# Optimization experiments

Measured on AMD Instinct MI355X. Metric: run time of the kernel, lower is better.

Reference implementation:

```python
import jax, jax.numpy as jnp
import numpy as np

B, S, H, NH = 2, 2048, 1024, 16
HD = H // NH  # head_dim = 64


def setup_inputs() -> dict:
    key = jax.random.key(0)
    kx, kl, kq, kk, kv, ko = jax.random.split(key, 6)
    scale = 1.0 / np.sqrt(H)
    return {
        "x": jax.random.normal(kx, (B, S, H), dtype=jnp.float32),
        "seq_lengths": jax.random.randint(kl, (B,), 1, S + 1, dtype=jnp.int32),
        "Wq": jax.random.normal(kq, (H, H), dtype=jnp.float32) * scale,
        "Wk": jax.random.normal(kk, (H, H), dtype=jnp.float32) * scale,
        "Wv": jax.random.normal(kv, (H, H), dtype=jnp.float32) * scale,
        "Wo": jax.random.normal(ko, (H, H), dtype=jnp.float32) * scale,
    }


def reference(x, seq_lengths, Wq, Wk, Wv, Wo):
    b, s, _ = x.shape
    # projections (nn.Linear with no bias: x @ W.T)
    q = (x @ Wq.T).reshape(b, s, NH, HD).transpose(0, 2, 1, 3)  # [b,h,s,d]
    k = (x @ Wk.T).reshape(b, s, NH, HD).transpose(0, 2, 1, 3)
    v = (x @ Wv.T).reshape(b, s, NH, HD).transpose(0, 2, 1, 3)

    scores = jnp.einsum("bhqd,bhkd->bhqk", q, k) / jnp.sqrt(jnp.float32(HD))

    causal = jnp.triu(jnp.ones((s, s), dtype=bool), k=1)[None, None]  # [1,1,s,s]
    padding = (jnp.arange(s)[None, :] >= seq_lengths[:, None])[:, None, None, :]
    mask = causal | padding
    scores = jnp.where(mask, -jnp.inf, scores)

    att = jax.nn.softmax(scores, axis=-1)  # stable: subtract row max once
    out = jnp.einsum("bhqk,bhkd->bhqd", att, v)
    out = out.transpose(0, 2, 1, 3).reshape(b, s, H)
    return out @ Wo.T
```

## Files before the change

### kernel.cpp

```cpp
#include <hip/hip_runtime.h>

typedef unsigned short u16;
typedef short bf16x8 __attribute__((ext_vector_type(8)));
typedef float f32x4 __attribute__((ext_vector_type(4)));

#define DEVINL __device__ __forceinline__

DEVINL u16 f2bf(float f) {
    union { float f; unsigned int u; } x;
    x.f = f;
    unsigned int u = x.u;
    unsigned int r = (u + 0x7fffu + ((u >> 16) & 1u)) >> 16;
    return (u16)r;
}

DEVINL unsigned int cvtpk(float a, float b) {
    unsigned int r;
    asm("v_cvt_pk_bf16_f32 %0, %1, %2" : "=v"(r) : "v"(a), "v"(b));
    return r;
}

DEVINL void async16(const u16* g, u16* l) {
    __builtin_amdgcn_global_load_lds(
        (const __attribute__((address_space(1))) void*)g,
        (__attribute__((address_space(3))) void*)l, 16, 0, 0);
}

DEVINL f32x4 mfma32(bf16x8 a, bf16x8 b, f32x4 c) {
    return __builtin_amdgcn_mfma_f32_16x16x32_bf16(a, b, c, 0, 0, 0);
}

__global__ void pma_cvt_all(const float* __restrict__ x,
                            const float* __restrict__ w0, const float* __restrict__ w1,
                            const float* __restrict__ w2, const float* __restrict__ w3,
                            u16* __restrict__ xb, u16* __restrict__ wdst) {
    const int y = blockIdx.y;
    const int i = blockIdx.x * 256 + threadIdx.x;
    const float4* src;
    ushort4* dst;
    float s = 1.0f;
    if (y < 4) {
        src = (const float4*)x + (size_t)y * 262144;
        dst = (ushort4*)xb + (size_t)y * 262144;
    } else {
        const int wsel = y - 4;
        const float* w = (wsel == 0) ? w0 : (wsel == 1) ? w1 : (wsel == 2) ? w2 : w3;
        src = (const float4*)w;
        dst = (ushort4*)wdst + (size_t)wsel * 262144;
        if (wsel == 0) s = 0.125f;
    }
    float4 v = src[i];
    ushort4 o;
    o.x = f2bf(v.x * s); o.y = f2bf(v.y * s); o.z = f2bf(v.z * s); o.w = f2bf(v.w * s);
    dst[i] = o;
}

__global__ __launch_bounds__(256) void pma_gemm_qkv(
    const u16* __restrict__ A,
    const u16* __restrict__ W0, const u16* __restrict__ W1, const u16* __restrict__ W2,
    u16* __restrict__ O0, u16* __restrict__ O1, u16* __restrict__ Vt,
    const int* __restrict__ seq_lengths)
{
    const int t = threadIdx.x;
    const int lane = t & 63, wave = t >> 6;
    const int m0 = blockIdx.x * 64;
    const int bn = blockIdx.y;
    const int which = bn >> 4;
    const int n0 = (bn & 15) * 64;

    if (which != 0 && (m0 & 2047) >= seq_lengths[m0 >> 11]) return;

    const u16* W = (which == 0) ? W0 : (which == 1) ? W1 : W2;

    __shared__ u16 Alds[64 * 64];
    __shared__ u16 Blds[64 * 64];

    const int wm = wave >> 1, wn = wave & 1;
    const int r16 = lane & 15, g4 = lane >> 4;
    const int r7 = r16 & 7;

    f32x4 acc[2][2];
    const f32x4 z = {0.f, 0.f, 0.f, 0.f};
#pragma unroll
    for (int m = 0; m < 2; ++m)
#pragma unroll
        for (int n = 0; n < 2; ++n) acc[m][n] = z;

    for (int k0 = 0; k0 < 1024; k0 += 64) {
        __syncthreads();
#pragma unroll
        for (int j = 0; j < 2; ++j) {
            int i = j * 256 + t;
            int row = i >> 3, seg = i & 7;
            int sc = ((seg ^ (row & 7)) * 8);
            async16(A + (size_t)(m0 + row) * 1024 + k0 + sc,
                    Alds + (size_t)(j * 256 + wave * 64) * 8);
            async16(W + (size_t)(n0 + row) * 1024 + k0 + sc,
                    Blds + (size_t)(j * 256 + wave * 64) * 8);
        }
        __syncthreads();

#pragma unroll
        for (int half = 0; half < 2; ++half) {
            bf16x8 af[2], bfr[2];
#pragma unroll
            for (int m = 0; m < 2; ++m)
                af[m] = *reinterpret_cast<const bf16x8*>(
                    Alds + (wm * 32 + m * 16 + r16) * 64 + (((half * 4 + g4) ^ r7) * 8));
#pragma unroll
            for (int n = 0; n < 2; ++n)
                bfr[n] = *reinterpret_cast<const bf16x8*>(
                    Blds + (wn * 32 + n * 16 + r16) * 64 + (((half * 4 + g4) ^ r7) * 8));
#pragma unroll
            for (int m = 0; m < 2; ++m)
#pragma unroll
                for (int n = 0; n < 2; ++n)
                    acc[m][n] = mfma32(af[m], bfr[n], acc[m][n]);
        }
    }

    if (which == 2) {
#pragma unroll
        for (int m = 0; m < 2; ++m)
#pragma unroll
            for (int n = 0; n < 2; ++n) {
                int row = m0 + wm * 32 + m * 16 + g4 * 4;
                int col = n0 + wn * 32 + n * 16 + r16;
                ushort4 pk;
                pk.x = f2bf(acc[m][n][0]); pk.y = f2bf(acc[m][n][1]);
                pk.z = f2bf(acc[m][n][2]); pk.w = f2bf(acc[m][n][3]);
                size_t addr = ((size_t)((row >> 11) * 16 + (col >> 6)) * 64 + (col & 63)) * 2048
                              + (row & 2047);
                *reinterpret_cast<ushort4*>(Vt + addr) = pk;
            }
    } else {
        u16* O = (which == 0) ? O0 : O1;
#pragma unroll
        for (int m = 0; m < 2; ++m)
#pragma unroll
            for (int n = 0; n < 2; ++n) {
                int row = m0 + wm * 32 + m * 16 + g4 * 4;
                int col = n0 + wn * 32 + n * 16 + r16;
#pragma unroll
                for (int r = 0; r < 4; ++r)
                    O[(size_t)(row + r) * 1024 + col] = f2bf(acc[m][n][r]);
            }
    }
}

__global__ __launch_bounds__(256) void pma_gemm_wo(
    const u16* __restrict__ A, const u16* __restrict__ W, float* __restrict__ O)
{
    const int t = threadIdx.x;
    const int lane = t & 63, wave = t >> 6;
    const int m0 = blockIdx.x * 64;
    const int n0 = blockIdx.y * 64;

    __shared__ u16 Alds[64 * 32];
    __shared__ u16 Blds[64 * 32];

    const int wm = wave >> 1, wn = wave & 1;
    const int r16 = lane & 15, g4 = lane >> 4;

    f32x4 acc[2][2];
    const f32x4 z = {0.f, 0.f, 0.f, 0.f};
#pragma unroll
    for (int m = 0; m < 2; ++m)
#pragma unroll
        for (int n = 0; n < 2; ++n) acc[m][n] = z;

    for (int k0 = 0; k0 < 1024; k0 += 32) {
        __syncthreads();
        {
            int row = t >> 2, seg = t & 3;
            async16(A + (size_t)(m0 + row) * 1024 + k0 + seg * 8,
                    Alds + (size_t)(wave * 64) * 8);
            async16(W + (size_t)(n0 + row) * 1024 + k0 + seg * 8,
                    Blds + (size_t)(wave * 64) * 8);
        }
        __syncthreads();

        bf16x8 af[2], bfr[2];
#pragma unroll
        for (int m = 0; m < 2; ++m)
            af[m] = *reinterpret_cast<const bf16x8*>(Alds + (wm * 32 + m * 16 + r16) * 32 + g4 * 8);
#pragma unroll
        for (int n = 0; n < 2; ++n)
            bfr[n] = *reinterpret_cast<const bf16x8*>(Blds + (wn * 32 + n * 16 + r16) * 32 + g4 * 8);
#pragma unroll
        for (int m = 0; m < 2; ++m)
#pragma unroll
            for (int n = 0; n < 2; ++n)
                acc[m][n] = mfma32(af[m], bfr[n], acc[m][n]);
    }

#pragma unroll
    for (int m = 0; m < 2; ++m)
#pragma unroll
        for (int n = 0; n < 2; ++n) {
            int row = m0 + wm * 32 + m * 16 + g4 * 4;
            int col = n0 + wn * 32 + n * 16 + r16;
#pragma unroll
            for (int r = 0; r < 4; ++r)
                O[(size_t)(row + r) * 1024 + col] = acc[m][n][r];
        }
}

__global__ __launch_bounds__(256, 4) void pma_attn_kernel(
    const u16* __restrict__ Q, const u16* __restrict__ Kp, const u16* __restrict__ Vt,
    const int* __restrict__ seq_lengths, u16* __restrict__ O)
{
    const int bx = blockIdx.x;
    const int qt = 31 - (bx >> 5);
    const int bh = bx & 31;
    const int h  = bh & 15;
    const int b  = bh >> 4;
    const int q0 = qt * 64;
    const int t = threadIdx.x, lane = t & 63, w = t >> 6;
    const int r16 = lane & 15, g4 = lane >> 4;
    const int seqlen = seq_lengths[b];
    const float L2E = 1.4426950408889634f;
    const float NB = 8.0f * L2E;

    __shared__ u16 Klds[2 * 64 * 64];
    __shared__ u16 Vlds[2 * 64 * 64];
    __shared__ u16 Plds[64 * 64];

    const size_t bbase = (size_t)b * 2048 * 1024;
    const size_t hoff = (size_t)h * 64;
    const size_t vrow0 = (size_t)((b * 16 + h) * 64);

    const f32x4 z = {0.f, 0.f, 0.f, 0.f};
    const int krel = t >> 3;
    const int seg  = t & 7;

    const size_t qrowbase = bbase + (size_t)(q0 + w * 16 + r16) * 1024 + hoff;
    const bf16x8 qf0 = *reinterpret_cast<const bf16x8*>(Q + qrowbase + g4 * 8);
    const bf16x8 qf1 = *reinterpret_cast<const bf16x8*>(Q + qrowbase + 32 + g4 * 8);

    bf16x8 vones;
#pragma unroll
    for (int j = 0; j < 8; ++j) vones[j] = (short)0x3F80;

    f32x4 acc[4], accL;
#pragma unroll
    for (int f = 0; f < 4; ++f) acc[f] = z;
    accL = z;

    int kmax = q0 + 63;
    if (seqlen - 1 < kmax) kmax = seqlen - 1;
    const int nt = (kmax >> 6) + 1;

    const u16* kbase = Kp + bbase + hoff + (size_t)krel * 1024 + seg * 8;
    const u16* vbase = Vt + (vrow0 + krel) * 2048 + seg * 8;
    const int stw = krel * 64 + ((seg ^ (krel & 7)) * 8);

    const int r7 = r16 & 7;
    const int kread_lo = r16 * 64 + ((g4 ^ r7) * 8);
    const int kread_hi = r16 * 64 + (((g4 + 4) ^ r7) * 8);
    const int prow = (w * 16 + r16) * 64;

    bf16x8 kreg[2], vreg[2];

#pragma unroll
    for (int j = 0; j < 2; ++j) {
        kreg[j] = *reinterpret_cast<const bf16x8*>(kbase + j * 32 * 1024);
        vreg[j] = *reinterpret_cast<const bf16x8*>(vbase + j * 32 * 2048);
    }
#pragma unroll
    for (int j = 0; j < 2; ++j) {
        *reinterpret_cast<bf16x8*>(Klds + stw + j * 2048) = kreg[j];
        *reinterpret_cast<bf16x8*>(Vlds + stw + j * 2048) = vreg[j];
    }
    __syncthreads();

    const int qhat = q0 + w * 16 + r16;

    for (int tt = 0; tt < nt; ++tt) {
        const int t0 = tt << 6;
        const int dbo = (tt & 1) << 12;
        const int dbn = 4096 - dbo;

        if (tt + 1 < nt) {
            const int t0n = (tt + 1) << 6;
#pragma unroll
            for (int j = 0; j < 2; ++j) {
                kreg[j] = *reinterpret_cast<const bf16x8*>(kbase + (size_t)t0n * 1024 + j * 32 * 1024);
                vreg[j] = *reinterpret_cast<const bf16x8*>(vbase + t0n + j * 32 * 2048);
            }
        }

        f32x4 sraw[4];
        __builtin_amdgcn_s_setprio(1);
#pragma unroll
        for (int kc = 0; kc < 4; ++kc) {
            bf16x8 kf0 = *reinterpret_cast<const bf16x8*>(Klds + dbo + kc * 1024 + kread_lo);
            bf16x8 kf1 = *reinterpret_cast<const bf16x8*>(Klds + dbo + kc * 1024 + kread_hi);
            f32x4 s = z;
            s = mfma32(kf0, qf0, s);
            s = mfma32(kf1, qf1, s);
            sraw[kc] = s;
        }
        __builtin_amdgcn_s_setprio(0);

        float sc[4][4];
        const bool needmask = (t0 == q0) || (t0 + 64 > seqlen);
#pragma unroll
        for (int kc = 0; kc < 4; ++kc)
#pragma unroll
            for (int r = 0; r < 4; ++r)
                sc[kc][r] = exp2f(__builtin_fmaf(sraw[kc][r], L2E, -NB));
        if (needmask) {
#pragma unroll
            for (int kc = 0; kc < 4; ++kc) {
                const int keyb = t0 + kc * 16 + g4 * 4;
#pragma unroll
                for (int r = 0; r < 4; ++r)
                    if ((keyb + r > qhat) || (keyb + r >= seqlen)) sc[kc][r] = 0.f;
            }
        }

#pragma unroll
        for (int kc = 0; kc < 4; ++kc) {
            uint2 pk;
            pk.x = cvtpk(sc[kc][0], sc[kc][1]);
            pk.y = cvtpk(sc[kc][2], sc[kc][3]);
            const int phys16 = (kc * 2 + (g4 >> 1)) ^ r7;
            *reinterpret_cast<uint2*>(Plds + prow + phys16 * 8 + (g4 & 1) * 4) = pk;
        }

        __builtin_amdgcn_s_setprio(1);
#pragma unroll
        for (int kc2 = 0; kc2 < 2; ++kc2) {
            bf16x8 pa = *reinterpret_cast<const bf16x8*>(Plds + prow + (((kc2 * 4 + g4) ^ r7) * 8));
            accL = mfma32(pa, vones, accL);
#pragma unroll
            for (int f = 0; f < 4; ++f) {
                bf16x8 vb = *reinterpret_cast<const bf16x8*>(
                    Vlds + dbo + (f * 16 + r16) * 64 + (((kc2 * 4 + g4) ^ r7) * 8));
                acc[f] = mfma32(pa, vb, acc[f]);
            }
        }
        __builtin_amdgcn_s_setprio(0);

        if (tt + 1 < nt) {
#pragma unroll
            for (int j = 0; j < 2; ++j) {
                *reinterpret_cast<bf16x8*>(Klds + dbn + stw + j * 2048) = kreg[j];
                *reinterpret_cast<bf16x8*>(Vlds + dbn + stw + j * 2048) = vreg[j];
            }
            __syncthreads();
        }
    }

#pragma unroll
    for (int f = 0; f < 4; ++f)
#pragma unroll
        for (int r = 0; r < 4; ++r) {
            int sr = q0 + w * 16 + g4 * 4 + r;
            float o = acc[f][r] / accL[r];
            O[bbase + (size_t)sr * 1024 + hoff + f * 16 + r16] = f2bf(o);
        }
}

extern "C" void kernel_launch(void* const* d_in, const int* in_sizes, int n_in,
                              void* d_out, int out_size, void* d_ws, size_t ws_size,
                              hipStream_t stream) {
    const float* x   = (const float*)d_in[0];
    const int*   sql = (const int*)d_in[1];
    const float* Wq  = (const float*)d_in[2];
    const float* Wk  = (const float*)d_in[3];
    const float* Wv  = (const float*)d_in[4];
    const float* Wo  = (const float*)d_in[5];
    float* out = (float*)d_out;

    const size_t MB = 1024 * 1024;
    char* ws = (char*)d_ws;
    u16* xb   = (u16*)(ws + 0 * MB);
    u16* wqb  = (u16*)(ws + 8 * MB);
    u16* wkb  = (u16*)(ws + 10 * MB);
    u16* wvb  = (u16*)(ws + 12 * MB);
    u16* wob  = (u16*)(ws + 14 * MB);
    u16* Qb   = (u16*)(ws + 16 * MB);
    u16* Kb   = (u16*)(ws + 24 * MB);
    u16* Vtb  = (u16*)(ws + 32 * MB);
    u16* attb = (u16*)(ws + 40 * MB);

    pma_cvt_all<<<dim3(1024, 8), 256, 0, stream>>>(x, Wq, Wk, Wv, Wo, xb, wqb);

    pma_gemm_qkv<<<dim3(64, 48), 256, 0, stream>>>(xb, wqb, wkb, wvb, Qb, Kb, Vtb, sql);

    pma_attn_kernel<<<1024, 256, 0, stream>>>(Qb, Kb, Vtb, sql, attb);

    pma_gemm_wo<<<dim3(64, 16), 256, 0, stream>>>(attb, wob, out);
}
```

Baseline: 102.5 us.

## Keep softmax probabilities in registers and use 16x16x16 MFMA for PV

Drops the shared-memory round trip for the probability tile. The score accumulator layout is fed directly as the A operand of v_mfma_f32_16x16x16_bf16, with matching V chunks read from LDS. This frees the P LDS buffer and raises the launch-bounds occupancy hint from 4 to 5 blocks. In exchange it issues twice as many smaller MFMAs, adds inline-asm s_nops for hazards, and the volatile asm may limit compiler scheduling.

```diff
diff --git a/kernel.cpp b/kernel.cpp
--- a/kernel.cpp
+++ b/kernel.cpp
@@ -2,6 +2,7 @@
 
 typedef unsigned short u16;
 typedef short bf16x8 __attribute__((ext_vector_type(8)));
+typedef short bf16x4 __attribute__((ext_vector_type(4)));
 typedef float f32x4 __attribute__((ext_vector_type(4)));
 
 #define DEVINL __device__ __forceinline__
@@ -28,6 +29,11 @@
 
 DEVINL f32x4 mfma32(bf16x8 a, bf16x8 b, f32x4 c) {
     return __builtin_amdgcn_mfma_f32_16x16x32_bf16(a, b, c, 0, 0, 0);
+}
+DEVINL f32x4 mfma16(bf16x4 a, bf16x4 b, f32x4 c) {
+    asm volatile("s_nop 1\n\tv_mfma_f32_16x16x16_bf16 %0, %1, %2, %0"
+                 : "+v"(c) : "v"(a), "v"(b));
+    return c;
 }
 
 __global__ void pma_cvt_all(const float* __restrict__ x,
@@ -206,7 +212,7 @@
         }
 }
 
-__global__ __launch_bounds__(256, 4) void pma_attn_kernel(
+__global__ __launch_bounds__(256, 5) void pma_attn_kernel(
     const u16* __restrict__ Q, const u16* __restrict__ Kp, const u16* __restrict__ Vt,
     const int* __restrict__ seq_lengths, u16* __restrict__ O)
 {
@@ -224,7 +230,6 @@
 
     __shared__ u16 Klds[2 * 64 * 64];
     __shared__ u16 Vlds[2 * 64 * 64];
-    __shared__ u16 Plds[64 * 64];
 
     const size_t bbase = (size_t)b * 2048 * 1024;
     const size_t hoff = (size_t)h * 64;
@@ -238,9 +243,9 @@
     const bf16x8 qf0 = *reinterpret_cast<const bf16x8*>(Q + qrowbase + g4 * 8);
     const bf16x8 qf1 = *reinterpret_cast<const bf16x8*>(Q + qrowbase + 32 + g4 * 8);
 
-    bf16x8 vones;
-#pragma unroll
-    for (int j = 0; j < 8; ++j) vones[j] = (short)0x3F80;
+    bf16x4 vones4;
+#pragma unroll
+    for (int j = 0; j < 4; ++j) vones4[j] = (short)0x3F80;
 
     f32x4 acc[4], accL;
 #pragma unroll
@@ -258,7 +263,6 @@
     const int r7 = r16 & 7;
     const int kread_lo = r16 * 64 + ((g4 ^ r7) * 8);
     const int kread_hi = r16 * 64 + (((g4 + 4) ^ r7) * 8);
-    const int prow = (w * 16 + r16) * 64;
 
     bf16x8 kreg[2], vreg[2];
 
@@ -320,26 +324,26 @@
             }
         }
 
+        bf16x4 pa[4];
 #pragma unroll
         for (int kc = 0; kc < 4; ++kc) {
-            uint2 pk;
-            pk.x = cvtpk(sc[kc][0], sc[kc][1]);
-            pk.y = cvtpk(sc[kc][2], sc[kc][3]);
-            const int phys16 = (kc * 2 + (g4 >> 1)) ^ r7;
-            *reinterpret_cast<uint2*>(Plds + prow + phys16 * 8 + (g4 & 1) * 4) = pk;
+            union { unsigned int u[2]; bf16x4 v; } pk;
+            pk.u[0] = cvtpk(sc[kc][0], sc[kc][1]);
+            pk.u[1] = cvtpk(sc[kc][2], sc[kc][3]);
+            pa[kc] = pk.v;
         }
 
         __builtin_amdgcn_s_setprio(1);
 #pragma unroll
-        for (int kc2 = 0; kc2 < 2; ++kc2) {
-            bf16x8 pa = *reinterpret_cast<const bf16x8*>(Plds + prow + (((kc2 * 4 + g4) ^ r7) * 8));
-            accL = mfma32(pa, vones, accL);
+        for (int kc = 0; kc < 4; ++kc) {
+            const int vchunk = (((kc * 2 + (g4 >> 1)) ^ r7) * 8) + (g4 & 1) * 4;
 #pragma unroll
             for (int f = 0; f < 4; ++f) {
-                bf16x8 vb = *reinterpret_cast<const bf16x8*>(
-                    Vlds + dbo + (f * 16 + r16) * 64 + (((kc2 * 4 + g4) ^ r7) * 8));
-                acc[f] = mfma32(pa, vb, acc[f]);
-            }
+                bf16x4 vb = *reinterpret_cast<const bf16x4*>(
+                    Vlds + dbo + (f * 16 + r16) * 64 + vchunk);
+                acc[f] = mfma16(pa[kc], vb, acc[f]);
+            }
+            accL = mfma16(pa[kc], vones4, accL);
         }
         __builtin_amdgcn_s_setprio(0);
 
@@ -353,6 +357,7 @@
         }
     }
 
+    asm volatile("s_nop 7\n\ts_nop 7");
 #pragma unroll
     for (int f = 0; f < 4; ++f)
 #pragma unroll
```

Result: slower. 111.3 us (+8.6%).
